# Performance work log

Hardware: AMD Instinct MI355X
Metric: run time of the kernel (lower is better)

## Reference

```python
import jax, jax.numpy as jnp
import numpy as np

B, T, D, H = 2, 2048, 1024, 16
HD = D // H
REG = 16
WIN = 256
ROPE_BASE = 10000.0


def _rope_cos_sin(t, hd):
    theta = 1.0 / (ROPE_BASE ** (jnp.arange(0, hd, 2, dtype=jnp.float32) / hd))  # [hd/2]
    idx_theta = jnp.arange(t, dtype=jnp.float32)[:, None] * theta[None, :]       # [T, hd/2]
    return jnp.cos(idx_theta), jnp.sin(idx_theta)


def _apply_rope(x, cos, sin):
    # x: [B, T, H, HD]
    xs = x.reshape(*x.shape[:-1], HD // 2, 2)
    x0, x1 = xs[..., 0], xs[..., 1]
    c = cos[None, :, None, :]
    s = sin[None, :, None, :]
    out = jnp.stack([x0 * c - x1 * s, x1 * c + x0 * s], axis=-1)
    return out.reshape(x.shape)


def _keep_mask(t):
    # Faithful to _build_attention_register_mask: True = attend (SDPA bool semantics).
    i = jnp.arange(t)[:, None]
    j = jnp.arange(t)[None, :]
    half = WIN // 2
    window_block = (i >= REG) & (j >= jnp.maximum(REG, i - half)) & (j <= i + half)
    blocked = (j < REG) | (i < REG) | window_block
    return ~blocked  # [T, T] bool


def setup_inputs() -> dict:
    key = jax.random.key(0)
    k1, k2, k3 = jax.random.split(key, 3)
    x = jax.random.normal(k1, (B, T, D), dtype=jnp.float32)
    w_attn = jax.random.normal(k2, (3 * D, D), dtype=jnp.float32) * 0.02  # torch Linear weight [out,in]
    w_proj = jax.random.normal(k3, (D, D), dtype=jnp.float32) * 0.02
    return {"x": x, "w_attn": w_attn, "w_proj": w_proj}


def reference(x, w_attn, w_proj):
    b, t, d = x.shape
    qkv = jnp.einsum('btd,ed->bte', x, w_attn)               # [B,T,3D]
    q, k, v = jnp.split(qkv, 3, axis=-1)
    q = q.reshape(b, t, H, HD)
    k = k.reshape(b, t, H, HD)
    v = v.reshape(b, t, H, HD)
    cos, sin = _rope_cos_sin(t, HD)
    q = _apply_rope(q, cos, sin)
    k = _apply_rope(k, cos, sin)
    q = q.transpose(0, 2, 1, 3)  # [B,H,T,HD]
    k = k.transpose(0, 2, 1, 3)
    v = v.transpose(0, 2, 1, 3)
    keep = _keep_mask(t)
    scores = jnp.einsum('bhqd,bhkd->bhqk', q, k) / jnp.sqrt(jnp.float32(HD))
    scores = jnp.where(keep[None, None], scores, -jnp.inf)
    # safe softmax (fully-masked rows -> 0, matching SDPA efficient backends)
    m = jnp.max(scores, axis=-1, keepdims=True)
    m = jnp.where(jnp.isfinite(m), m, 0.0)
    e = jnp.exp(scores - m)
    s = jnp.sum(e, axis=-1, keepdims=True)
    probs = e / jnp.maximum(s, 1e-20)
    y = jnp.einsum('bhqk,bhkd->bhqd', probs, v)
    y = y.transpose(0, 2, 1, 3).reshape(b, t, d)
    return jnp.einsum('btd,ed->bte', y, w_proj)
```

## Files before the change

### kernel.cpp

```cpp
#include <hip/hip_runtime.h>
#include <hip/hip_bf16.h>

#define DEV static __device__ __forceinline__

typedef __attribute__((ext_vector_type(8))) short bf16x8;
typedef __attribute__((ext_vector_type(4))) short bf16x4;
typedef __attribute__((ext_vector_type(4))) float f32x4;

#define MFMA16(a, b, c) __builtin_amdgcn_mfma_f32_16x16x32_bf16((a), (b), (c), 0, 0, 0)

DEV f32x4 pv_mfma(bf16x4 a, bf16x4 b, f32x4 c) {
#if __has_builtin(__builtin_amdgcn_mfma_f32_16x16x16_bf16)
  return __builtin_amdgcn_mfma_f32_16x16x16_bf16(a, b, c, 0, 0, 0);
#elif __has_builtin(__builtin_amdgcn_mfma_f32_16x16x16bf16_1k)
  return __builtin_amdgcn_mfma_f32_16x16x16bf16_1k(a, b, c, 0, 0, 0);
#else
  f32x4 d;
  asm volatile("v_mfma_f32_16x16x16_bf16 %0, %1, %2, %3"
               : "=v"(d) : "v"(a), "v"(b), "v"(c));
  return d;
#endif
}

#define B_ 2
#define T_ 2048
#define D_ 1024
#define H_ 16
#define HD_ 64
#define LOG2E 1.4426950408889634f

DEV short f2bf(float f) {
  union { float f; unsigned u; } w; w.f = f;
  unsigned u = w.u + 0x7fffu + ((w.u >> 16) & 1u);
  return (short)(u >> 16);
}

DEV void gld16(const void* g, void* l) {
  __builtin_amdgcn_global_load_lds(
      (const __attribute__((address_space(1))) void*)g,
      (__attribute__((address_space(3))) void*)l, 16, 0, 0);
}

#define XN 4194304
#define WAN 3145728
__global__ void cvt_k(const float* __restrict__ x, const float* __restrict__ wa,
                      const float* __restrict__ wp, short* __restrict__ xb,
                      short* __restrict__ wab, short* __restrict__ wpb) {
  size_t gi = ((size_t)blockIdx.x * 256 + threadIdx.x) * 8;
  const float* src; short* dst;
  if (gi < XN) { src = x + gi; dst = xb + gi; }
  else if (gi < XN + WAN) { src = wa + (gi - XN); dst = wab + (gi - XN); }
  else { src = wp + (gi - XN - WAN); dst = wpb + (gi - XN - WAN); }
  float4 a = *(const float4*)src;
  float4 b = *(const float4*)(src + 4);
  bf16x8 o;
  o[0] = f2bf(a.x); o[1] = f2bf(a.y); o[2] = f2bf(a.z); o[3] = f2bf(a.w);
  o[4] = f2bf(b.x); o[5] = f2bf(b.y); o[6] = f2bf(b.z); o[7] = f2bf(b.w);
  *(bf16x8*)dst = o;
}

__global__ void rope_table_k(float2* __restrict__ tab) {
  int i = blockIdx.x * 256 + threadIdx.x;
  if (i >= T_ * 32) return;
  int t = i >> 5, d = i & 31;
  float theta = powf(10000.0f, -(float)(2 * d) / 64.0f);
  float a = (float)t * theta;
  tab[i] = make_float2(cosf(a), sinf(a));
}

#define GEMM_CORE(Aptr, Bptr, KDIM)                                              \
  __shared__ short aT[128 * 64];                                                 \
  __shared__ short bT[128 * 64];                                                 \
  const int tid = threadIdx.x;                                                   \
  const int lane = tid & 63, w = tid >> 6;                                       \
  const int l15 = lane & 15, lg = lane >> 4;                                     \
  const int wr = w >> 1, wc = w & 1;                                             \
  const int mBase = blockIdx.y * 128, nBase = blockIdx.x * 128;                  \
  const int lrow = lane >> 3;                                                    \
  const int gch = (lane & 7) ^ lrow;                                             \
  const short* Asrc = (Aptr) + (size_t)(mBase + w * 32 + lrow) * (KDIM) + gch * 8;\
  const short* Bsrc = (Bptr) + (size_t)(nBase + w * 32 + lrow) * (KDIM) + gch * 8;\
  short* aDst = aT + w * 2048;                                                   \
  short* bDst = bT + w * 2048;                                                   \
  f32x4 acc[4][4];                                                               \
  _Pragma("unroll") for (int i = 0; i < 4; ++i)                                  \
  _Pragma("unroll") for (int j = 0; j < 4; ++j)                                  \
      acc[i][j] = (f32x4){0.f, 0.f, 0.f, 0.f};                                   \
  const int nk = (KDIM) / 64;                                                    \
  for (int kt = 0; kt < nk; ++kt) {                                              \
    if (kt) __syncthreads();                                                     \
    _Pragma("unroll") for (int p = 0; p < 4; ++p) {                              \
      gld16(Asrc + kt * 64 + p * 8 * (KDIM), aDst + p * 512);                    \
      gld16(Bsrc + kt * 64 + p * 8 * (KDIM), bDst + p * 512);                    \
    }                                                                            \
    __syncthreads();                \
    bf16x8 af[4][2], bfv[4][2];                                                  \
    _Pragma("unroll") for (int i = 0; i < 4; ++i)                                \
    _Pragma("unroll") for (int s = 0; s < 2; ++s) {                              \
      const int ra = wr * 64 + i * 16 + l15;                                     \
      const int rb = wc * 64 + i * 16 + l15;                                     \
      af[i][s] = *(const bf16x8*)&aT[ra * 64 + (((4 * s + lg) ^ (ra & 7)) * 8)]; \
      bfv[i][s] = *(const bf16x8*)&bT[rb * 64 + (((4 * s + lg) ^ (rb & 7)) * 8)];\
    }                                                                            \
    _Pragma("unroll") for (int mi = 0; mi < 4; ++mi)                             \
    _Pragma("unroll") for (int ni = 0; ni < 4; ++ni)                             \
    _Pragma("unroll") for (int s = 0; s < 2; ++s)                                \
        acc[mi][ni] = MFMA16(af[mi][s], bfv[ni][s], acc[mi][ni]);                \
  }

__global__ void gemm_qkv_k(const short* __restrict__ Xb, const short* __restrict__ Wb,
                           short* __restrict__ Q, short* __restrict__ Ko,
                           short* __restrict__ Vt, const float2* __restrict__ tab) {
  GEMM_CORE(Xb, Wb, 1024)

  const int sec = nBase >> 10;
#pragma unroll
  for (int mi = 0; mi < 4; ++mi) {
    const int m0 = mBase + wr * 64 + mi * 16 + lg * 4;
#pragma unroll
    for (int ni = 0; ni < 4; ++ni) {
      const int n = nBase + wc * 64 + ni * 16 + l15;
      const int hd = n & 63;
      const int h = (n >> 6) & 15;
      if (sec < 2) {
        short* dst = (sec == 0) ? Q : Ko;
        const float qscale = (sec == 0) ? (0.125f * LOG2E) : 1.0f;
#pragma unroll
        for (int r = 0; r < 4; ++r) {
          int m = m0 + r; int b = m >> 11; int t = m & 2047;
          float v = acc[mi][ni][r];
          float pv = __shfl_xor(v, 1);
          float2 cs = tab[t * 32 + (hd >> 1)];
          float o = (lane & 1) ? (v * cs.x + pv * cs.y) : (v * cs.x - pv * cs.y);
          o *= qscale;
          dst[(((size_t)b * H_ + h) * T_ + t) * HD_ + hd] = f2bf(o);
        }
      } else {
        int b = m0 >> 11; int t0 = m0 & 2047;
        short4 s4;
        s4.x = f2bf(acc[mi][ni][0]); s4.y = f2bf(acc[mi][ni][1]);
        s4.z = f2bf(acc[mi][ni][2]); s4.w = f2bf(acc[mi][ni][3]);
        *(short4*)&Vt[(((size_t)b * H_ + h) * HD_ + hd) * T_ + t0] = s4;
      }
    }
  }
}

__global__ __launch_bounds__(256, 4) void attn_k(const short* __restrict__ Qg,
                                                 const short* __restrict__ Kg,
                                                 const short* __restrict__ Vg,
                                                 short* __restrict__ Y) {
  __shared__ short kLds[64 * 72];
  __shared__ short vLds[64 * 72];
  const int tid = threadIdx.x;
  const int lane = tid & 63, w = tid >> 6;
  const int l15 = lane & 15, lg = lane >> 4;
  const int bid = blockIdx.x;
  const int wg = ((bid & 7) << 7) | (bid >> 3);
  const int qt = wg & 31, bh = wg >> 5;
  const int b = bh >> 4, h = bh & 15;
  const int q0 = qt * 64;
  const short* Qh = Qg + (size_t)bh * T_ * HD_;
  const short* Kh = Kg + (size_t)bh * T_ * HD_;
  const short* Vh = Vg + (size_t)bh * HD_ * T_;

  bf16x8 qb[2];
  {
    const int qrow = q0 + w * 16 + l15;
    qb[0] = *(const bf16x8*)&Qh[(size_t)qrow * HD_ + lg * 8];
    qb[1] = *(const bf16x8*)&Qh[(size_t)qrow * HD_ + 32 + lg * 8];
  }
  f32x4 ot[4];
#pragma unroll
  for (int i = 0; i < 4; ++i) ot[i] = (f32x4){0.f, 0.f, 0.f, 0.f};
  float lsum = 0.f;

  const int sRow = tid >> 3, sC = (tid & 7) * 8;
  bf16x8 kreg[2], vreg[2];
  auto issueLoad = [&](int kt) {
    const int k0 = kt * 64;
#pragma unroll
    for (int p = 0; p < 2; ++p) {
      const int row = sRow + p * 32;
      kreg[p] = *(const bf16x8*)&Kh[(size_t)(k0 + row) * HD_ + sC];
      vreg[p] = *(const bf16x8*)&Vh[(size_t)row * T_ + k0 + sC];
    }
  };
  auto inBand = [&](int kt) { const int k0 = kt * 64; return k0 >= q0 - 65 && k0 <= q0 + 65; };

  const int NT = T_ / 64;
  int kt = 0;
  while (kt < NT && inBand(kt)) ++kt;
  issueLoad(kt);

  while (kt < NT) {
    int ktn = kt + 1;
    while (ktn < NT && inBand(ktn)) ++ktn;

    __syncthreads();
#pragma unroll
    for (int p = 0; p < 2; ++p) {
      const int row = sRow + p * 32;
      *(bf16x8*)&kLds[row * 72 + (((tid & 7) ^ (row & 7)) * 8)] = kreg[p];
      *(bf16x8*)&vLds[row * 72 + sC] = vreg[p];
    }
    if (ktn < NT) issueLoad(ktn);
    asm volatile("s_waitcnt lgkmcnt(0)" ::: "memory");
    __builtin_amdgcn_s_barrier();

    const int k0 = kt * 64;
    const bool clean = (q0 >= 16) && (k0 >= 16) &&
                       ((k0 + 63 < q0 - 128) || (k0 > q0 + 63 + 128));

    f32x4 s[4];
#pragma unroll
    for (int i = 0; i < 4; ++i) s[i] = (f32x4){0.f, 0.f, 0.f, 0.f};
    __builtin_amdgcn_s_setprio(1);
#pragma unroll
    for (int nf = 0; nf < 4; ++nf)
#pragma unroll
      for (int ks = 0; ks < 2; ++ks) {
        const int row = nf * 16 + l15;
        bf16x8 ka = *(const bf16x8*)&kLds[row * 72 + (((ks * 4 + lg) ^ (row & 7)) * 8)];
        s[nf] = MFMA16(ka, qb[ks], s[nf]);
      }
    __builtin_amdgcn_s_setprio(0);

    const int i_q = q0 + w * 16 + l15;
    bf16x4 pf[4];
#pragma unroll
    for (int nf = 0; nf < 4; ++nf)
#pragma unroll
      for (int r = 0; r < 4; ++r) {
        if (!clean) {
          const int j = k0 + nf * 16 + lg * 4 + r;
          const bool keep = (i_q >= 16) && (j >= 16) &&
                            ((j < i_q - 128) || (j > i_q + 128));
          if (!keep) s[nf][r] = -__builtin_inff();
        }
        float e = __builtin_amdgcn_exp2f(s[nf][r]);
        lsum += e;
        pf[nf][r] = f2bf(e);
      }

    __builtin_amdgcn_s_setprio(1);
#pragma unroll
    for (int kk = 0; kk < 4; ++kk) {
      bf16x4 va[4];
#pragma unroll
      for (int dt = 0; dt < 4; ++dt)
        va[dt] = *(const bf16x4*)&vLds[(dt * 16 + l15) * 72 + kk * 16 + lg * 4];
#pragma unroll
      for (int dt = 0; dt < 4; ++dt)
        ot[dt] = pv_mfma(va[dt], pf[kk], ot[dt]);
    }
    __builtin_amdgcn_s_setprio(0);
    kt = ktn;
  }

  float l = lsum;
  l += __shfl_xor(l, 16);
  l += __shfl_xor(l, 32);
  const float rl = 1.0f / fmaxf(l, 1e-20f);

  __syncthreads();
  short* tl = kLds + w * (16 * 72);
#pragma unroll
  for (int dt = 0; dt < 4; ++dt) {
    short4 s4;
    s4.x = f2bf(ot[dt][0] * rl);
    s4.y = f2bf(ot[dt][1] * rl);
    s4.z = f2bf(ot[dt][2] * rl);
    s4.w = f2bf(ot[dt][3] * rl);
    *(short4*)&tl[l15 * 72 + dt * 16 + lg * 4] = s4;
  }
  const int rr = lane >> 3, cc = (lane & 7) * 8;
#pragma unroll
  for (int hf = 0; hf < 2; ++hf) {
    const int row = hf * 8 + rr;
    bf16x8 v = *(const bf16x8*)&tl[row * 72 + cc];
    const int t = q0 + w * 16 + row;
    *(bf16x8*)&Y[((size_t)(b * T_ + t)) * D_ + h * HD_ + cc] = v;
  }
}

__global__ void gemm_proj_k(const short* __restrict__ Yg, const short* __restrict__ Wb,
                            float* __restrict__ Out) {
  GEMM_CORE(Yg, Wb, 1024)

#pragma unroll
  for (int mi = 0; mi < 4; ++mi)
#pragma unroll
    for (int ni = 0; ni < 4; ++ni)
#pragma unroll
      for (int r = 0; r < 4; ++r)
        Out[(size_t)(mBase + wr * 64 + mi * 16 + lg * 4 + r) * 1024 +
            nBase + wc * 64 + ni * 16 + l15] = acc[mi][ni][r];
}

extern "C" void kernel_launch(void* const* d_in, const int* in_sizes, int n_in,
                              void* d_out, int out_size, void* d_ws, size_t ws_size,
                              hipStream_t stream) {
  const float* x = (const float*)d_in[0];
  const float* w_attn = (const float*)d_in[1];
  const float* w_proj = (const float*)d_in[2];
  float* out = (float*)d_out;
  char* ws = (char*)d_ws;
  char* outc = (char*)d_out;
  short* Q   = (short*)(ws);
  short* K   = (short*)(ws + (size_t)8388608);
  short* Vt  = (short*)(ws + (size_t)16777216);
  short* Y   = (short*)(ws + (size_t)25165824);
  short* Wpb = (short*)(ws + (size_t)33554432);
  short* Xb   = (short*)(outc);
  short* Wab  = (short*)(outc + (size_t)8388608);
  float2* tab = (float2*)(outc + (size_t)14680064);

  cvt_k<<<dim3(4096), dim3(256), 0, stream>>>(x, w_attn, w_proj, Xb, Wab, Wpb);
  rope_table_k<<<dim3(256), dim3(256), 0, stream>>>(tab);
  gemm_qkv_k<<<dim3(24, 32), dim3(256), 0, stream>>>(Xb, Wab, Q, K, Vt, tab);
  attn_k<<<dim3(B_ * H_ * (T_ / 64)), dim3(256), 0, stream>>>(Q, K, Vt, Y);
  gemm_proj_k<<<dim3(8, 32), dim3(256), 0, stream>>>(Y, Wpb, out);
}
```

Measured before the change: 149.3 us.

## Process key tiles in pairs of 128 with new LDS layouts and packed bf16 convert

The attention loop now stages 128 keys per barrier instead of 64, halving the number of sync points and doubling the loads in flight per iteration. K and V get new conflict-avoiding LDS layouts (K split by column chunk, V interleaved by 4-key groups). Any 64-key half that falls in the excluded band is skipped. The softmax conversion to bf16 now uses the hardware v_cvt_pk_bf16_f32 instruction in place of manual rounding. In exchange, register use and LDS footprint grow, which may reduce occupancy, and the band-skip is now coarser.

```diff
diff --git a/kernel.cpp b/kernel.cpp
--- a/kernel.cpp
+++ b/kernel.cpp
@@ -20,6 +20,15 @@
                : "=v"(d) : "v"(a), "v"(b), "v"(c));
   return d;
 #endif
+}
+
+DEV bf16x4 pk4(float e0, float e1, float e2, float e3) {
+  unsigned lo, hi;
+  asm("v_cvt_pk_bf16_f32 %0, %1, %2" : "=v"(lo) : "v"(e0), "v"(e1));
+  asm("v_cvt_pk_bf16_f32 %0, %1, %2" : "=v"(hi) : "v"(e2), "v"(e3));
+  union { unsigned u[2]; bf16x4 v; } r;
+  r.u[0] = lo; r.u[1] = hi;
+  return r.v;
 }
 
 #define B_ 2
@@ -146,12 +155,13 @@
   }
 }
 
+#define NPAIR 16
 __global__ __launch_bounds__(256, 4) void attn_k(const short* __restrict__ Qg,
                                                  const short* __restrict__ Kg,
                                                  const short* __restrict__ Vg,
                                                  short* __restrict__ Y) {
-  __shared__ short kLds[64 * 72];
-  __shared__ short vLds[64 * 72];
+  __shared__ short kLds[8 * 128 * 8];
+  __shared__ short vLds[32 * 264];
   const int tid = threadIdx.x;
   const int lane = tid & 63, w = tid >> 6;
   const int l15 = lane & 15, lg = lane >> 4;
@@ -175,87 +185,107 @@
   for (int i = 0; i < 4; ++i) ot[i] = (f32x4){0.f, 0.f, 0.f, 0.f};
   float lsum = 0.f;
 
-  const int sRow = tid >> 3, sC = (tid & 7) * 8;
-  bf16x8 kreg[2], vreg[2];
-  auto issueLoad = [&](int kt) {
-    const int k0 = kt * 64;
-#pragma unroll
-    for (int p = 0; p < 2; ++p) {
-      const int row = sRow + p * 32;
-      kreg[p] = *(const bf16x8*)&Kh[(size_t)(k0 + row) * HD_ + sC];
-      vreg[p] = *(const bf16x8*)&Vh[(size_t)row * T_ + k0 + sC];
+  const int kRow = tid >> 3, kC = tid & 7;
+  const int vD = tid >> 4, vC = tid & 15;
+  bf16x8 kreg[4], vreg[4];
+  auto issueLoad = [&](int k0) {
+#pragma unroll
+    for (int p = 0; p < 4; ++p)
+      kreg[p] = *(const bf16x8*)&Kh[(size_t)(k0 + kRow + p * 32) * HD_ + kC * 8];
+#pragma unroll
+    for (int p = 0; p < 4; ++p)
+      vreg[p] = *(const bf16x8*)&Vh[(size_t)(vD + p * 16) * T_ + k0 + vC * 8];
+  };
+  auto stage = [&]() {
+#pragma unroll
+    for (int p = 0; p < 4; ++p)
+      *(bf16x8*)&kLds[kC * 1024 + (kRow + p * 32) * 8] = kreg[p];
+#pragma unroll
+    for (int p = 0; p < 4; ++p) {
+      const int d = vD + p * 16;
+      bf16x4 lo = {vreg[p][0], vreg[p][1], vreg[p][2], vreg[p][3]};
+      bf16x4 hi = {vreg[p][4], vreg[p][5], vreg[p][6], vreg[p][7]};
+      *(bf16x4*)&vLds[(2 * vC) * 264 + d * 4] = lo;
+      *(bf16x4*)&vLds[(2 * vC + 1) * 264 + d * 4] = hi;
     }
   };
-  auto inBand = [&](int kt) { const int k0 = kt * 64; return k0 >= q0 - 65 && k0 <= q0 + 65; };
-
-  const int NT = T_ / 64;
-  int kt = 0;
-  while (kt < NT && inBand(kt)) ++kt;
-  issueLoad(kt);
-
-  while (kt < NT) {
-    int ktn = kt + 1;
-    while (ktn < NT && inBand(ktn)) ++ktn;
+  auto halfBanned = [&](int kh) { return kh >= q0 - 65 && kh <= q0 + 65; };
+  auto pairSkip = [&](int kp) {
+    const int k0 = kp * 128;
+    return halfBanned(k0) && halfBanned(k0 + 64);
+  };
+
+  int kp = 0;
+  while (kp < NPAIR && pairSkip(kp)) ++kp;
+  issueLoad(kp * 128);
+
+  const int i_q = q0 + w * 16 + l15;
+
+  while (kp < NPAIR) {
+    int kpn = kp + 1;
+    while (kpn < NPAIR && pairSkip(kpn)) ++kpn;
 
     __syncthreads();
-#pragma unroll
-    for (int p = 0; p < 2; ++p) {
-      const int row = sRow + p * 32;
-      *(bf16x8*)&kLds[row * 72 + (((tid & 7) ^ (row & 7)) * 8)] = kreg[p];
-      *(bf16x8*)&vLds[row * 72 + sC] = vreg[p];
-    }
-    if (ktn < NT) issueLoad(ktn);
+    stage();
+    if (kpn < NPAIR) issueLoad(kpn * 128);
     asm volatile("s_waitcnt lgkmcnt(0)" ::: "memory");
     __builtin_amdgcn_s_barrier();
 
-    const int k0 = kt * 64;
-    const bool clean = (q0 >= 16) && (k0 >= 16) &&
-                       ((k0 + 63 < q0 - 128) || (k0 > q0 + 63 + 128));
-
-    f32x4 s[4];
-#pragma unroll
-    for (int i = 0; i < 4; ++i) s[i] = (f32x4){0.f, 0.f, 0.f, 0.f};
-    __builtin_amdgcn_s_setprio(1);
-#pragma unroll
-    for (int nf = 0; nf < 4; ++nf)
-#pragma unroll
-      for (int ks = 0; ks < 2; ++ks) {
-        const int row = nf * 16 + l15;
-        bf16x8 ka = *(const bf16x8*)&kLds[row * 72 + (((ks * 4 + lg) ^ (row & 7)) * 8)];
-        s[nf] = MFMA16(ka, qb[ks], s[nf]);
+    const int k0 = kp * 128;
+#pragma unroll
+    for (int hv = 0; hv < 2; ++hv) {
+      const int kh = k0 + hv * 64;
+      if (halfBanned(kh)) continue;
+      const bool clean = (q0 >= 16) && (kh >= 16) &&
+                         ((kh + 63 < q0 - 128) || (kh > q0 + 63 + 128));
+
+      f32x4 s[4];
+#pragma unroll
+      for (int i = 0; i < 4; ++i) s[i] = (f32x4){0.f, 0.f, 0.f, 0.f};
+      __builtin_amdgcn_s_setprio(1);
+#pragma unroll
+      for (int nf = 0; nf < 4; ++nf)
+#pragma unroll
+        for (int ks = 0; ks < 2; ++ks) {
+          bf16x8 ka = *(const bf16x8*)
+              &kLds[(ks * 4 + lg) * 1024 + (hv * 64 + nf * 16 + l15) * 8];
+          s[nf] = MFMA16(ka, qb[ks], s[nf]);
+        }
+      __builtin_amdgcn_s_setprio(0);
+
+      bf16x4 pf[4];
+#pragma unroll
+      for (int nf = 0; nf < 4; ++nf) {
+        float e[4];
+#pragma unroll
+        for (int r = 0; r < 4; ++r) {
+          if (!clean) {
+            const int j = kh + nf * 16 + lg * 4 + r;
+            const bool keep = (i_q >= 16) && (j >= 16) &&
+                              ((j < i_q - 128) || (j > i_q + 128));
+            if (!keep) s[nf][r] = -__builtin_inff();
+          }
+          e[r] = __builtin_amdgcn_exp2f(s[nf][r]);
+          lsum += e[r];
+        }
+        pf[nf] = pk4(e[0], e[1], e[2], e[3]);
       }
-    __builtin_amdgcn_s_setprio(0);
-
-    const int i_q = q0 + w * 16 + l15;
-    bf16x4 pf[4];
-#pragma unroll
-    for (int nf = 0; nf < 4; ++nf)
-#pragma unroll
-      for (int r = 0; r < 4; ++r) {
-        if (!clean) {
-          const int j = k0 + nf * 16 + lg * 4 + r;
-          const bool keep = (i_q >= 16) && (j >= 16) &&
-                            ((j < i_q - 128) || (j > i_q + 128));
-          if (!keep) s[nf][r] = -__builtin_inff();
-        }
-        float e = __builtin_amdgcn_exp2f(s[nf][r]);
-        lsum += e;
-        pf[nf][r] = f2bf(e);
+
+      __builtin_amdgcn_s_setprio(1);
+#pragma unroll
+      for (int kk = 0; kk < 4; ++kk) {
+        bf16x4 va[4];
+#pragma unroll
+        for (int dt = 0; dt < 4; ++dt)
+          va[dt] = *(const bf16x4*)
+              &vLds[(hv * 16 + kk * 4 + lg) * 264 + (dt * 16 + l15) * 4];
+#pragma unroll
+        for (int dt = 0; dt < 4; ++dt)
+          ot[dt] = pv_mfma(va[dt], pf[kk], ot[dt]);
       }
-
-    __builtin_amdgcn_s_setprio(1);
-#pragma unroll
-    for (int kk = 0; kk < 4; ++kk) {
-      bf16x4 va[4];
-#pragma unroll
-      for (int dt = 0; dt < 4; ++dt)
-        va[dt] = *(const bf16x4*)&vLds[(dt * 16 + l15) * 72 + kk * 16 + lg * 4];
-#pragma unroll
-      for (int dt = 0; dt < 4; ++dt)
-        ot[dt] = pv_mfma(va[dt], pf[kk], ot[dt]);
+      __builtin_amdgcn_s_setprio(0);
     }
-    __builtin_amdgcn_s_setprio(0);
-    kt = ktn;
+    kp = kpn;
   }
 
   float l = lsum;
```

New measurement: 156.5 us. 4.8% more time.

## Share K/V tiles across two 64-query groups per block with packed bf16 convert

Applied to the files above, without the earlier changes.

The attention block grows from 256 to 512 threads and covers 128 queries as two 64-query wave groups that share each K/V tile staged in LDS. This halves global K/V loads and barriers per query. Tiles inside the local window are skipped per group, and only tiles banned for both groups are skipped for the whole block. It also packs the exp results to bf16 with v_cvt_pk_bf16_f32 and drops the XOR swizzle on the K LDS tile, which may cause bank conflicts. The output staging now indexes past kLds into the adjacent vLds region, so it relies on the two LDS arrays being contiguous.

```diff
diff --git a/kernel.cpp b/kernel.cpp
--- a/kernel.cpp
+++ b/kernel.cpp
@@ -20,6 +20,15 @@
                : "=v"(d) : "v"(a), "v"(b), "v"(c));
   return d;
 #endif
+}
+
+DEV bf16x4 pk4(float e0, float e1, float e2, float e3) {
+  unsigned lo, hi;
+  asm("v_cvt_pk_bf16_f32 %0, %1, %2" : "=v"(lo) : "v"(e0), "v"(e1));
+  asm("v_cvt_pk_bf16_f32 %0, %1, %2" : "=v"(hi) : "v"(e2), "v"(e3));
+  union { unsigned u[2]; bf16x4 v; } r;
+  r.u[0] = lo; r.u[1] = hi;
+  return r.v;
 }
 
 #define B_ 2
@@ -146,7 +155,8 @@
   }
 }
 
-__global__ __launch_bounds__(256, 4) void attn_k(const short* __restrict__ Qg,
+#define QBLK 128
+__global__ __launch_bounds__(512, 4) void attn_k(const short* __restrict__ Qg,
                                                  const short* __restrict__ Kg,
                                                  const short* __restrict__ Vg,
                                                  short* __restrict__ Y) {
@@ -154,107 +164,102 @@
   __shared__ short vLds[64 * 72];
   const int tid = threadIdx.x;
   const int lane = tid & 63, w = tid >> 6;
+  const int g = w >> 2, wl = w & 3;
   const int l15 = lane & 15, lg = lane >> 4;
   const int bid = blockIdx.x;
-  const int wg = ((bid & 7) << 7) | (bid >> 3);
-  const int qt = wg & 31, bh = wg >> 5;
+  const int wg = ((bid & 7) << 6) | (bid >> 3);
+  const int qt = wg & 15, bh = wg >> 4;
   const int b = bh >> 4, h = bh & 15;
-  const int q0 = qt * 64;
+  const int q0 = qt * QBLK;
+  const int qg = q0 + g * 64;
   const short* Qh = Qg + (size_t)bh * T_ * HD_;
   const short* Kh = Kg + (size_t)bh * T_ * HD_;
   const short* Vh = Vg + (size_t)bh * HD_ * T_;
 
+  const int qrow = qg + wl * 16 + l15;
   bf16x8 qb[2];
-  {
-    const int qrow = q0 + w * 16 + l15;
-    qb[0] = *(const bf16x8*)&Qh[(size_t)qrow * HD_ + lg * 8];
-    qb[1] = *(const bf16x8*)&Qh[(size_t)qrow * HD_ + 32 + lg * 8];
-  }
+  qb[0] = *(const bf16x8*)&Qh[(size_t)qrow * HD_ + lg * 8];
+  qb[1] = *(const bf16x8*)&Qh[(size_t)qrow * HD_ + 32 + lg * 8];
+
   f32x4 ot[4];
 #pragma unroll
   for (int i = 0; i < 4; ++i) ot[i] = (f32x4){0.f, 0.f, 0.f, 0.f};
   float lsum = 0.f;
 
   const int sRow = tid >> 3, sC = (tid & 7) * 8;
-  bf16x8 kreg[2], vreg[2];
+  bf16x8 kreg, vreg;
   auto issueLoad = [&](int kt) {
     const int k0 = kt * 64;
-#pragma unroll
-    for (int p = 0; p < 2; ++p) {
-      const int row = sRow + p * 32;
-      kreg[p] = *(const bf16x8*)&Kh[(size_t)(k0 + row) * HD_ + sC];
-      vreg[p] = *(const bf16x8*)&Vh[(size_t)row * T_ + k0 + sC];
-    }
+    kreg = *(const bf16x8*)&Kh[(size_t)(k0 + sRow) * HD_ + sC];
+    vreg = *(const bf16x8*)&Vh[(size_t)sRow * T_ + k0 + sC];
   };
-  auto inBand = [&](int kt) { const int k0 = kt * 64; return k0 >= q0 - 65 && k0 <= q0 + 65; };
+  auto bothBanned = [&](int kt) { const int k0 = kt * 64; return k0 >= q0 - 1 && k0 <= q0 + 65; };
 
   const int NT = T_ / 64;
   int kt = 0;
-  while (kt < NT && inBand(kt)) ++kt;
+  while (kt < NT && bothBanned(kt)) ++kt;
   issueLoad(kt);
 
   while (kt < NT) {
     int ktn = kt + 1;
-    while (ktn < NT && inBand(ktn)) ++ktn;
+    while (ktn < NT && bothBanned(ktn)) ++ktn;
 
     __syncthreads();
-#pragma unroll
-    for (int p = 0; p < 2; ++p) {
-      const int row = sRow + p * 32;
-      *(bf16x8*)&kLds[row * 72 + (((tid & 7) ^ (row & 7)) * 8)] = kreg[p];
-      *(bf16x8*)&vLds[row * 72 + sC] = vreg[p];
-    }
+    *(bf16x8*)&kLds[sRow * 72 + sC] = kreg;
+    *(bf16x8*)&vLds[sRow * 72 + sC] = vreg;
     if (ktn < NT) issueLoad(ktn);
     asm volatile("s_waitcnt lgkmcnt(0)" ::: "memory");
     __builtin_amdgcn_s_barrier();
 
     const int k0 = kt * 64;
-    const bool clean = (q0 >= 16) && (k0 >= 16) &&
-                       ((k0 + 63 < q0 - 128) || (k0 > q0 + 63 + 128));
-
-    f32x4 s[4];
-#pragma unroll
-    for (int i = 0; i < 4; ++i) s[i] = (f32x4){0.f, 0.f, 0.f, 0.f};
-    __builtin_amdgcn_s_setprio(1);
-#pragma unroll
-    for (int nf = 0; nf < 4; ++nf)
-#pragma unroll
-      for (int ks = 0; ks < 2; ++ks) {
-        const int row = nf * 16 + l15;
-        bf16x8 ka = *(const bf16x8*)&kLds[row * 72 + (((ks * 4 + lg) ^ (row & 7)) * 8)];
-        s[nf] = MFMA16(ka, qb[ks], s[nf]);
+    if (!(k0 >= qg - 65 && k0 <= qg + 65)) {
+      const bool clean = (qg >= 16) && (k0 >= 16) &&
+                         ((k0 + 63 < qg - 128) || (k0 > qg + 63 + 128));
+
+      f32x4 s[4];
+#pragma unroll
+      for (int i = 0; i < 4; ++i) s[i] = (f32x4){0.f, 0.f, 0.f, 0.f};
+      __builtin_amdgcn_s_setprio(1);
+#pragma unroll
+      for (int nf = 0; nf < 4; ++nf)
+#pragma unroll
+        for (int ks = 0; ks < 2; ++ks) {
+          bf16x8 ka = *(const bf16x8*)&kLds[(nf * 16 + l15) * 72 + ks * 32 + lg * 8];
+          s[nf] = MFMA16(ka, qb[ks], s[nf]);
+        }
+      __builtin_amdgcn_s_setprio(0);
+
+      bf16x4 pf[4];
+#pragma unroll
+      for (int nf = 0; nf < 4; ++nf) {
+        float e[4];
+#pragma unroll
+        for (int r = 0; r < 4; ++r) {
+          if (!clean) {
+            const int j = k0 + nf * 16 + lg * 4 + r;
+            const bool keep = (qrow >= 16) && (j >= 16) &&
+                              ((j < qrow - 128) || (j > qrow + 128));
+            if (!keep) s[nf][r] = -__builtin_inff();
+          }
+          e[r] = __builtin_amdgcn_exp2f(s[nf][r]);
+          lsum += e[r];
+        }
+        pf[nf] = pk4(e[0], e[1], e[2], e[3]);
       }
-    __builtin_amdgcn_s_setprio(0);
-
-    const int i_q = q0 + w * 16 + l15;
-    bf16x4 pf[4];
-#pragma unroll
-    for (int nf = 0; nf < 4; ++nf)
-#pragma unroll
-      for (int r = 0; r < 4; ++r) {
-        if (!clean) {
-          const int j = k0 + nf * 16 + lg * 4 + r;
-          const bool keep = (i_q >= 16) && (j >= 16) &&
-                            ((j < i_q - 128) || (j > i_q + 128));
-          if (!keep) s[nf][r] = -__builtin_inff();
-        }
-        float e = __builtin_amdgcn_exp2f(s[nf][r]);
-        lsum += e;
-        pf[nf][r] = f2bf(e);
+
+      __builtin_amdgcn_s_setprio(1);
+#pragma unroll
+      for (int kk = 0; kk < 4; ++kk) {
+        bf16x4 va[4];
+#pragma unroll
+        for (int dt = 0; dt < 4; ++dt)
+          va[dt] = *(const bf16x4*)&vLds[(dt * 16 + l15) * 72 + kk * 16 + lg * 4];
+#pragma unroll
+        for (int dt = 0; dt < 4; ++dt)
+          ot[dt] = pv_mfma(va[dt], pf[kk], ot[dt]);
       }
-
-    __builtin_amdgcn_s_setprio(1);
-#pragma unroll
-    for (int kk = 0; kk < 4; ++kk) {
-      bf16x4 va[4];
-#pragma unroll
-      for (int dt = 0; dt < 4; ++dt)
-        va[dt] = *(const bf16x4*)&vLds[(dt * 16 + l15) * 72 + kk * 16 + lg * 4];
-#pragma unroll
-      for (int dt = 0; dt < 4; ++dt)
-        ot[dt] = pv_mfma(va[dt], pf[kk], ot[dt]);
+      __builtin_amdgcn_s_setprio(0);
     }
-    __builtin_amdgcn_s_setprio(0);
     kt = ktn;
   }
 
@@ -279,7 +284,7 @@
   for (int hf = 0; hf < 2; ++hf) {
     const int row = hf * 8 + rr;
     bf16x8 v = *(const bf16x8*)&tl[row * 72 + cc];
-    const int t = q0 + w * 16 + row;
+    const int t = qg + wl * 16 + row;
     *(bf16x8*)&Y[((size_t)(b * T_ + t)) * D_ + h * HD_ + cc] = v;
   }
 }
@@ -319,6 +324,6 @@
   cvt_k<<<dim3(4096), dim3(256), 0, stream>>>(x, w_attn, w_proj, Xb, Wab, Wpb);
   rope_table_k<<<dim3(256), dim3(256), 0, stream>>>(tab);
   gemm_qkv_k<<<dim3(24, 32), dim3(256), 0, stream>>>(Xb, Wab, Q, K, Vt, tab);
-  attn_k<<<dim3(B_ * H_ * (T_ / 64)), dim3(256), 0, stream>>>(Q, K, Vt, Y);
+  attn_k<<<dim3(B_ * H_ * (T_ / QBLK)), dim3(512), 0, stream>>>(Q, K, Vt, Y);
   gemm_proj_k<<<dim3(8, 32), dim3(256), 0, stream>>>(Y, Wpb, out);
 }
```

Measured after the change: 132.9 us. 1.12x faster.
